# Performance work log

Hardware: AMD Instinct MI355X
Metric: run time of the kernel (lower is better)

## Reference

```python
import jax, jax.numpy as jnp
import numpy as np

N_HEAD_HALF = 8          # config.n_head // 2
LAMBDA_INIT = 0.2        # diff_lambda_init
RMS_EPS = 1.1920929e-07  # torch.finfo(float32).eps (F.rms_norm default)
ROPE_BASE = 10000.0


def setup_inputs() -> dict:
    key = jax.random.key(0)
    ks = jax.random.split(key, 9)
    B, T, C = 2, 2048, 2048
    HD = C // N_HEAD_HALF  # 256
    s = 0.02
    return {
        "x": jax.random.normal(ks[0], (B, T, C), jnp.float32),
        "wq": jax.random.normal(ks[1], (C, C), jnp.float32) * s,
        "wk": jax.random.normal(ks[2], (C, C), jnp.float32) * s,
        "wv": jax.random.normal(ks[3], (C, C), jnp.float32) * s,
        "wo": jax.random.normal(ks[4], (C, C), jnp.float32) * s,
        "lq1": jax.random.normal(ks[5], (HD,), jnp.float32) * 0.1,
        "lk1": jax.random.normal(ks[6], (HD,), jnp.float32) * 0.1,
        "lq2": jax.random.normal(ks[7], (HD,), jnp.float32) * 0.1,
        "lk2": jax.random.normal(ks[8], (HD,), jnp.float32) * 0.1,
    }


def _rms_norm(x):
    var = jnp.mean(x * x, axis=-1, keepdims=True)
    return x * jax.lax.rsqrt(var + RMS_EPS)


def _rotary(x):
    # Faithful to original bug: positions run along axis 1 (the HEAD axis),
    # since Rotary is applied after transpose(1,2). x: (B, NH, T, D)
    d = x.shape[-1]
    inv_freq = (1.0 / ROPE_BASE) ** (jnp.arange(0, d, 2, dtype=jnp.float32) / d)
    t = jnp.arange(x.shape[1], dtype=jnp.float32)
    freqs = jnp.outer(t, inv_freq)                      # (NH, d/2)
    cos = jnp.cos(freqs)[None, :, None, :]
    sin = jnp.sin(freqs)[None, :, None, :]
    x1, x2 = jnp.split(x, 2, axis=-1)
    return jnp.concatenate((x1 * cos + x2 * sin, -x1 * sin + x2 * cos), axis=-1)


def _causal_attn(q, k, v, scale):
    # q,k: (B,NH,T,Dh)  v: (B,NH,T,HD)
    T = q.shape[2]
    s = jnp.einsum("bhqd,bhkd->bhqk", q, k) * scale
    mask = jnp.tril(jnp.ones((T, T), dtype=bool))
    s = jnp.where(mask, s, jnp.float32(-jnp.inf))
    p = jax.nn.softmax(s, axis=-1)
    return jnp.einsum("bhqk,bhkd->bhqd", p, v)


def reference(x, wq, wk, wv, wo, lq1, lk1, lq2, lk2):
    B, T, C = x.shape
    NH = N_HEAD_HALF
    HD = C // NH
    HH = HD // 2

    lam1 = jnp.exp(jnp.sum(lq1 * lk1))
    lam2 = jnp.exp(jnp.sum(lq2 * lk2))
    lam = lam1 - lam2 + LAMBDA_INIT

    q = (x @ wq.T).reshape(B, T, NH, 2, HH).transpose(0, 2, 1, 3, 4)
    k = (x @ wk.T).reshape(B, T, NH, 2, HH).transpose(0, 2, 1, 3, 4)
    v = (x @ wv.T).reshape(B, T, NH, HD).transpose(0, 2, 1, 3)

    q1 = _rotary(_rms_norm(q[..., 0, :]))
    q2 = _rotary(_rms_norm(q[..., 1, :]))
    k1 = _rotary(_rms_norm(k[..., 0, :]))
    k2 = _rotary(_rms_norm(k[..., 1, :]))

    scale = 1.0 / jnp.sqrt(jnp.float32(HH))
    y = _causal_attn(q1, k1, v, scale) - lam * _causal_attn(q2, k2, v, scale)

    y = y.transpose(0, 2, 1, 3).reshape(B, T, C)
    y = (y @ wo.T) * (1.0 - LAMBDA_INIT)
    return y
```

## Files before the change

### kernel.cpp

```cpp
#include <hip/hip_runtime.h>
#include <hip/hip_bf16.h>

using bf16 = __hip_bfloat16;
typedef __bf16 bf16x8_t __attribute__((ext_vector_type(8)));
typedef __bf16 bf16x4_t __attribute__((ext_vector_type(4)));
typedef float f32x4  __attribute__((ext_vector_type(4)));
typedef float f32x16 __attribute__((ext_vector_type(16)));

#define AS1 __attribute__((address_space(1)))
#define AS3 __attribute__((address_space(3)))

__device__ __forceinline__ void gll16(const void* g, void* l) {
  __builtin_amdgcn_global_load_lds((const AS1 void*)g, (AS3 void*)l, 16u, 0, 0u);
}

__device__ __forceinline__ __bf16 tobf(float f) {
  bf16 h = __float2bfloat16(f);
  return __builtin_bit_cast(__bf16, h);
}

__global__ __launch_bounds__(256) void k_cvt(
    const float* __restrict__ x,  const float* __restrict__ wq,
    const float* __restrict__ wk, const float* __restrict__ wv,
    const float* __restrict__ wo,
    bf16* __restrict__ xb,  bf16* __restrict__ wqb, bf16* __restrict__ wkb,
    bf16* __restrict__ wvb, bf16* __restrict__ wob) {
  size_t id = (size_t)blockIdx.x * 256 + threadIdx.x;
  const float* s; bf16* d; size_t off;
  if (id < 2097152) { s = x; d = xb; off = id; }
  else {
    size_t r = id - 2097152;
    unsigned w = (unsigned)(r >> 20);
    off = r & 1048575u;
    s = (w == 0) ? wq : (w == 1) ? wk : (w == 2) ? wv : wo;
    d = (w == 0) ? wqb : (w == 1) ? wkb : (w == 2) ? wvb : wob;
  }
  const float4 v = ((const float4*)s)[off];
  bf16x4_t o = { tobf(v.x), tobf(v.y), tobf(v.z), tobf(v.w) };
  *(bf16x4_t*)(d + off * 4) = o;
}

__global__ __launch_bounds__(256) void k_lam(
    const float* __restrict__ lq1, const float* __restrict__ lk1,
    const float* __restrict__ lq2, const float* __restrict__ lk2,
    float* __restrict__ lam) {
  __shared__ float r1[4], r2[4];
  int t = threadIdx.x;
  float a = lq1[t] * lk1[t];
  float b = lq2[t] * lk2[t];
#pragma unroll
  for (int s = 1; s < 64; s <<= 1) { a += __shfl_xor(a, s); b += __shfl_xor(b, s); }
  if ((t & 63) == 0) { r1[t >> 6] = a; r2[t >> 6] = b; }
  __syncthreads();
  if (t == 0) {
    float s1 = r1[0] + r1[1] + r1[2] + r1[3];
    float s2 = r2[0] + r2[1] + r2[2] + r2[3];
    *lam = expf(s1) - expf(s2) + 0.2f;
  }
}

template<bool SWAP>
__device__ __forceinline__ void gemm_core(
    const bf16* __restrict__ A, const bf16* __restrict__ Bm,
    int m0, int n0, bf16* lA, bf16* lB, f32x4 (&acc)[4][4]) {
  const int tid  = threadIdx.x;
  const int lane = tid & 63;
  const int g    = lane >> 4;
  const int l15  = lane & 15;
  const int l7   = lane & 7;
  const int wave = tid >> 6;
  const int wm   = (wave >> 1) * 64;
  const int wn   = (wave & 1) * 64;

  int srow[4], ssc[4];
#pragma unroll
  for (int j = 0; j < 4; ++j) {
    int id = tid + j * 256;
    srow[j] = id >> 3;
    ssc[j]  = (id & 7) ^ (srow[j] & 7);
  }

  for (int k0 = 0; k0 < 2048; k0 += 64) {
    __syncthreads();
#pragma unroll
    for (int j = 0; j < 4; ++j) {
      int id = tid + j * 256;
      gll16(A  + (size_t)(m0 + srow[j]) * 2048 + k0 + ssc[j] * 8, lA + id * 8);
      gll16(Bm + (size_t)(n0 + srow[j]) * 2048 + k0 + ssc[j] * 8, lB + id * 8);
    }
    __syncthreads();
#pragma unroll
    for (int ks = 0; ks < 2; ++ks) {
      const int pc = (ks * 4 + g) ^ l7;
      bf16x8_t af[4], bfr[4];
#pragma unroll
      for (int mt = 0; mt < 4; ++mt)
        af[mt] = *(const bf16x8_t*)(lA + (wm + mt * 16 + l15) * 64 + pc * 8);
#pragma unroll
      for (int nt = 0; nt < 4; ++nt)
        bfr[nt] = *(const bf16x8_t*)(lB + (wn + nt * 16 + l15) * 64 + pc * 8);
#pragma unroll
      for (int mt = 0; mt < 4; ++mt)
#pragma unroll
        for (int nt = 0; nt < 4; ++nt) {
          if (SWAP)
            acc[mt][nt] = __builtin_amdgcn_mfma_f32_16x16x32_bf16(
                bfr[nt], af[mt], acc[mt][nt], 0, 0, 0);
          else
            acc[mt][nt] = __builtin_amdgcn_mfma_f32_16x16x32_bf16(
                af[mt], bfr[nt], acc[mt][nt], 0, 0, 0);
        }
    }
  }
}

__global__ __launch_bounds__(256) void k_gemm_qkv(
    const bf16* __restrict__ xb,
    const bf16* __restrict__ wqb, const bf16* __restrict__ wkb,
    const bf16* __restrict__ wvb,
    bf16* __restrict__ q1, bf16* __restrict__ q2,
    bf16* __restrict__ k1, bf16* __restrict__ k2,
    bf16* __restrict__ vt) {
  __shared__ __align__(16) bf16 lA[128 * 64];
  __shared__ __align__(16) bf16 lB[128 * 64];
  __shared__ float lCs[64], lSn[64];
  const int z  = blockIdx.z;
  const int m0 = blockIdx.y * 128, n0 = blockIdx.x * 128;
  const int tid = threadIdx.x;
  const int lane = tid & 63, wave = tid >> 6;
  const int g = lane >> 4, l15 = lane & 15, l7 = lane & 7;

  if (z < 2) {
    const bf16* Bm = z ? wkb : wqb;
    f32x4 acc[2][8] = {};

    int srow[4], ssc[4];
#pragma unroll
    for (int j = 0; j < 4; ++j) {
      int id = tid + j * 256;
      srow[j] = id >> 3;
      ssc[j]  = (id & 7) ^ (srow[j] & 7);
    }
    for (int k0 = 0; k0 < 2048; k0 += 64) {
      __syncthreads();
#pragma unroll
      for (int j = 0; j < 4; ++j) {
        int id = tid + j * 256;
        gll16(xb + (size_t)(m0 + srow[j]) * 2048 + k0 + ssc[j] * 8, lA + id * 8);
        gll16(Bm + (size_t)(n0 + srow[j]) * 2048 + k0 + ssc[j] * 8, lB + id * 8);
      }
      __syncthreads();
#pragma unroll
      for (int ks = 0; ks < 2; ++ks) {
        const int pc = (ks * 4 + g) ^ l7;
        bf16x8_t af[2], bfr[8];
#pragma unroll
        for (int mt = 0; mt < 2; ++mt)
          af[mt] = *(const bf16x8_t*)(lA + (wave * 32 + mt * 16 + l15) * 64 + pc * 8);
#pragma unroll
        for (int nt = 0; nt < 8; ++nt)
          bfr[nt] = *(const bf16x8_t*)(lB + (nt * 16 + l15) * 64 + pc * 8);
#pragma unroll
        for (int mt = 0; mt < 2; ++mt)
#pragma unroll
          for (int nt = 0; nt < 8; ++nt)
            acc[mt][nt] = __builtin_amdgcn_mfma_f32_16x16x32_bf16(
                bfr[nt], af[mt], acc[mt][nt], 0, 0, 0);
      }
    }

    const int nh = n0 >> 8, p = (n0 >> 7) & 1;
    __syncthreads();
    if (tid < 64) {
      float fr = exp2f(-(float)tid * 0.20762050593045951f);
      float sn, cs;
      sincosf((float)nh * fr, &sn, &cs);
      lCs[tid] = cs; lSn[tid] = sn;
    }
    __syncthreads();
    bf16* dst = z ? (p ? k2 : k1) : (p ? q2 : q1);
#pragma unroll
    for (int mt = 0; mt < 2; ++mt) {
      float ss = 0.f;
#pragma unroll
      for (int nt = 0; nt < 8; ++nt)
#pragma unroll
        for (int r = 0; r < 4; ++r) ss += acc[mt][nt][r] * acc[mt][nt][r];
      ss += __shfl_xor(ss, 16);
      ss += __shfl_xor(ss, 32);
      const float inv = rsqrtf(ss * (1.0f / 128.0f) + 1.1920929e-07f);
      const int tok = m0 + wave * 32 + mt * 16 + l15;
      const size_t base = ((size_t)tok * 8 + nh) * 128;
#pragma unroll
      for (int nt4 = 0; nt4 < 4; ++nt4) {
        const int jb = nt4 * 16 + 4 * g;
        bf16x4_t o1v, o2v;
#pragma unroll
        for (int r = 0; r < 4; ++r) {
          float cs = lCs[jb + r], sn = lSn[jb + r];
          float x1 = acc[mt][nt4][r] * inv;
          float x2 = acc[mt][nt4 + 4][r] * inv;
          o1v[r] = tobf(x1 * cs + x2 * sn);
          o2v[r] = tobf(x2 * cs - x1 * sn);
        }
        *(bf16x4_t*)(dst + base + jb)      = o1v;
        *(bf16x4_t*)(dst + base + jb + 64) = o2v;
      }
    }
  } else {
    f32x4 acc[4][4] = {};
    gemm_core<false>(xb, wvb, m0, n0, lA, lB, acc);
    const int wm = (wave >> 1) * 64, wn = (wave & 1) * 64;
#pragma unroll
    for (int mt = 0; mt < 4; ++mt)
#pragma unroll
      for (int nt = 0; nt < 4; ++nt) {
        int rb  = m0 + wm + mt * 16 + 4 * g;
        int col = n0 + wn + nt * 16 + l15;
        int nh = col >> 8, hd = col & 255;
        int b = rb >> 11, t = rb & 2047;
        bf16x4_t pv;
#pragma unroll
        for (int r = 0; r < 4; ++r) pv[r] = tobf(acc[mt][nt][r]);
        *(bf16x4_t*)(vt + ((size_t)((b * 8 + nh) * 256 + hd)) * 2048 + t) = pv;
      }
  }
}

__global__ __launch_bounds__(256) void k_gemm_out(
    const bf16* __restrict__ yb, const bf16* __restrict__ wob,
    float* __restrict__ outp) {
  __shared__ __align__(16) bf16 lA[128 * 64];
  __shared__ __align__(16) bf16 lB[128 * 64];
  const int m0 = blockIdx.y * 128, n0 = blockIdx.x * 128;
  f32x4 acc[4][4] = {};
  gemm_core<true>(yb, wob, m0, n0, lA, lB, acc);
  const int lane = threadIdx.x & 63, wave = threadIdx.x >> 6;
  const int g = lane >> 4, l15 = lane & 15;
  const int wm = (wave >> 1) * 64, wn = (wave & 1) * 64;
#pragma unroll
  for (int mt = 0; mt < 4; ++mt)
#pragma unroll
    for (int nt = 0; nt < 4; ++nt) {
      int row = m0 + wm + mt * 16 + l15;
      int col = n0 + wn + nt * 16 + 4 * g;
      f32x4 v;
#pragma unroll
      for (int r = 0; r < 4; ++r) v[r] = acc[mt][nt][r] * 0.8f;
      *(f32x4*)(outp + (size_t)row * 2048 + col) = v;
    }
}

__global__ __launch_bounds__(256, 1) void k_flash(
    const bf16* __restrict__ q1b, const bf16* __restrict__ q2b,
    const bf16* __restrict__ k1b, const bf16* __restrict__ k2b,
    const bf16* __restrict__ vtb, const float* __restrict__ lamp,
    bf16* __restrict__ yb) {
  __shared__ __align__(16) bf16 smem[65536];
  const int tid  = threadIdx.x;
  const int lane = tid & 63, wave = tid >> 6;
  const int pair = blockIdx.x;
  const int bh = blockIdx.y;
  const int b = bh >> 3, nh = bh & 7;
  const int at = wave & 1, qg = wave >> 1;
  const int l31 = lane & 31, g5 = lane >> 5, l7 = lane & 7;
  const float scale = 0.08838834764831845f;
  const float lam = *lamp;

  auto stage = [&](int kt, int buf) {
    bf16* dst = smem + buf * 32768;
    const int k0 = kt * 64;
#pragma unroll
    for (int it = 0; it < 4; ++it) {
      int id = tid + it * 256;
      int row = id >> 4, c = id & 15;
      int sc = (c & 8) | ((c & 7) ^ (row & 7));
      size_t goff = ((size_t)(b * 2048 + k0 + row) * 8 + nh) * 128 + sc * 8;
      gll16(k1b + goff, dst + id * 8);
      gll16(k2b + goff, dst + 8192 + id * 8);
    }
#pragma unroll
    for (int it = 0; it < 8; ++it) {
      int id = tid + it * 256;
      int row = id >> 3, c = id & 7;
      int sc = c ^ (row & 7);
      gll16(vtb + ((size_t)(bh * 256 + row)) * 2048 + k0 + sc * 8,
            dst + 16384 + id * 8);
    }
  };

  bf16x8_t qf[8];
  auto loadQ = [&](int qt) {
    int qglob = qt * 64 + qg * 32 + l31;
    const bf16* qp = (at ? q2b : q1b) +
                     ((size_t)(b * 2048 + qglob) * 8 + nh) * 128 + g5 * 8;
#pragma unroll
    for (int ks = 0; ks < 8; ++ks) qf[ks] = *(const bf16x8_t*)(qp + ks * 16);
  };

  f32x16 O[8];
  float mrun, lrun;
  auto resetO = [&]() {
#pragma unroll
    for (int i = 0; i < 8; ++i)
#pragma unroll
      for (int j = 0; j < 16; ++j) O[i][j] = 0.f;
    mrun = -1e30f; lrun = 0.f;
  };

  auto step = [&](int kt, int buf, int qt) {
    const bf16* lk = smem + buf * 32768 + (at ? 8192 : 0);
    const bf16* lv = smem + buf * 32768 + 16384;
    const int k0 = kt * 64;
    const int qglob = qt * 64 + qg * 32 + l31;

    f32x16 s0, s1;
#pragma unroll
    for (int j = 0; j < 16; ++j) { s0[j] = 0.f; s1[j] = 0.f; }
#pragma unroll
    for (int ks = 0; ks < 8; ++ks) {
      int cl = ks * 2 + g5;
      int pc = (cl & 8) | ((cl & 7) ^ l7);
      bf16x8_t a0 = *(const bf16x8_t*)(lk + l31 * 128 + pc * 8);
      bf16x8_t a1 = *(const bf16x8_t*)(lk + (32 + l31) * 128 + pc * 8);
      s0 = __builtin_amdgcn_mfma_f32_32x32x16_bf16(a0, qf[ks], s0, 0, 0, 0);
      s1 = __builtin_amdgcn_mfma_f32_32x32x16_bf16(a1, qf[ks], s1, 0, 0, 0);
    }

    const bool diag = (kt == qt);
    float rmax = -3.0e38f;
#pragma unroll
    for (int r = 0; r < 16; ++r) {
      int key0 = k0 + (r & 3) + 8 * (r >> 2) + 4 * g5;
      float v0 = s0[r] * scale;
      float v1 = s1[r] * scale;
      if (diag) {
        if (key0 > qglob)      v0 = -1e30f;
        if (key0 + 32 > qglob) v1 = -1e30f;
      }
      s0[r] = v0; s1[r] = v1;
      rmax = fmaxf(rmax, fmaxf(v0, v1));
    }
    rmax = fmaxf(rmax, __shfl_xor(rmax, 32));
    float mnew = fmaxf(mrun, rmax);
    float alpha = __expf(mrun - mnew);
    float psum = 0.f;
#pragma unroll
    for (int r = 0; r < 16; ++r) {
      float p0 = __expf(s0[r] - mnew);
      float p1 = __expf(s1[r] - mnew);
      s0[r] = p0; s1[r] = p1;
      psum += p0 + p1;
    }
    psum += __shfl_xor(psum, 32);
    lrun = lrun * alpha + psum;
    mrun = mnew;
#pragma unroll
    for (int i = 0; i < 8; ++i) O[i] *= alpha;

#pragma unroll
    for (int sl = 0; sl < 4; ++sl) {
      const int h = sl & 1;
      bf16x4_t lo, hi;
#pragma unroll
      for (int j = 0; j < 4; ++j) {
        float vl = (sl < 2) ? s0[h * 8 + j]     : s1[h * 8 + j];
        float vh = (sl < 2) ? s0[h * 8 + 4 + j] : s1[h * 8 + 4 + j];
        lo[j] = tobf(vl); hi[j] = tobf(vh);
      }
      bf16x4_t send = g5 ? lo : hi;
      int2 si = __builtin_bit_cast(int2, send);
      int2 ri;
      ri.x = __shfl_xor(si.x, 32);
      ri.y = __shfl_xor(si.y, 32);
      bf16x4_t recv = __builtin_bit_cast(bf16x4_t, ri);
      bf16x4_t f0 = g5 ? recv : lo;
      bf16x4_t f1 = g5 ? hi : recv;
      bf16x8_t pf = { f0[0], f0[1], f0[2], f0[3], f1[0], f1[1], f1[2], f1[3] };

      const int cl = sl * 2 + g5;
#pragma unroll
      for (int mt = 0; mt < 8; ++mt) {
        bf16x8_t vf = *(const bf16x8_t*)(lv + (mt * 32 + l31) * 64 + (cl ^ l7) * 8);
        O[mt] = __builtin_amdgcn_mfma_f32_32x32x16_bf16(vf, pf, O[mt], 0, 0, 0);
      }
    }
  };

  auto finish = [&](int qt, bf16* cb) {
    const int qglob = qt * 64 + qg * 32 + l31;
    const float invl = 1.f / lrun;
    __syncthreads();
    if (at) {
      const float f = lam * invl;
#pragma unroll
      for (int mt = 0; mt < 8; ++mt)
#pragma unroll
        for (int rq = 0; rq < 4; ++rq) {
          int hd = mt * 32 + 8 * rq + 4 * g5;
          bf16x4_t pv;
#pragma unroll
          for (int i = 0; i < 4; ++i) pv[i] = tobf(O[mt][rq * 4 + i] * f);
          *(bf16x4_t*)(cb + (size_t)(qg * 32 + l31) * 264 + hd) = pv;
        }
    }
    __syncthreads();
    if (!at) {
#pragma unroll
      for (int mt = 0; mt < 8; ++mt)
#pragma unroll
        for (int rq = 0; rq < 4; ++rq) {
          int hd = mt * 32 + 8 * rq + 4 * g5;
          bf16x4_t o2 = *(const bf16x4_t*)(cb + (size_t)(qg * 32 + l31) * 264 + hd);
          bf16x4_t pv;
#pragma unroll
          for (int i = 0; i < 4; ++i)
            pv[i] = tobf(O[mt][rq * 4 + i] * invl - (float)o2[i]);
          *(bf16x4_t*)(yb + (size_t)(b * 2048 + qglob) * 2048 + nh * 256 + hd) = pv;
        }
    }
  };

  const int qtB = 31 - pair, qtA = pair;

  loadQ(qtB);
  resetO();
  stage(0, 0);
  for (int kt = 0; kt <= qtB; ++kt) {
    __syncthreads();
    if (kt < qtB) stage(kt + 1, (kt + 1) & 1);
    else          stage(0, (kt + 1) & 1);
    step(kt, kt & 1, qtB);
  }
  finish(qtB, smem + (qtB & 1) * 32768);

  loadQ(qtA);
  resetO();
  for (int kt = 0; kt <= qtA; ++kt) {
    __syncthreads();
    if (kt < qtA) stage(kt + 1, (qtB + kt + 2) & 1);
    step(kt, (qtB + 1 + kt) & 1, qtA);
  }
  finish(qtA, smem + 32768);
}

extern "C" void kernel_launch(void* const* d_in, const int* in_sizes, int n_in,
                              void* d_out, int out_size, void* d_ws, size_t ws_size,
                              hipStream_t stream) {
  (void)in_sizes; (void)n_in; (void)out_size; (void)ws_size;
  const float* x   = (const float*)d_in[0];
  const float* wq  = (const float*)d_in[1];
  const float* wk  = (const float*)d_in[2];
  const float* wv  = (const float*)d_in[3];
  const float* wo  = (const float*)d_in[4];
  const float* lq1 = (const float*)d_in[5];
  const float* lk1 = (const float*)d_in[6];
  const float* lq2 = (const float*)d_in[7];
  const float* lk2 = (const float*)d_in[8];
  float* out = (float*)d_out;

  char* p = (char*)d_ws;
  float* lam = (float*)p;            p += 256;
  bf16* xb  = (bf16*)p;              p += (size_t)4096 * 2048 * 2;
  bf16* wqb = (bf16*)p;              p += (size_t)2048 * 2048 * 2;
  bf16* wkb = (bf16*)p;              p += (size_t)2048 * 2048 * 2;
  bf16* wvb = (bf16*)p;              p += (size_t)2048 * 2048 * 2;
  bf16* wob = (bf16*)p;              p += (size_t)2048 * 2048 * 2;
  bf16* vt  = (bf16*)p;              p += (size_t)4096 * 2048 * 2;
  bf16* q1b = (bf16*)p;              p += (size_t)4096 * 1024 * 2;
  bf16* q2b = (bf16*)p;              p += (size_t)4096 * 1024 * 2;
  bf16* k1b = (bf16*)p;              p += (size_t)4096 * 1024 * 2;
  bf16* k2b = (bf16*)p;              p += (size_t)4096 * 1024 * 2;
  bf16* yb  = (bf16*)p;              p += (size_t)4096 * 2048 * 2;

  k_cvt<<<24576, 256, 0, stream>>>(x, wq, wk, wv, wo, xb, wqb, wkb, wvb, wob);
  k_lam<<<1, 256, 0, stream>>>(lq1, lk1, lq2, lk2, lam);
  k_gemm_qkv<<<dim3(16, 32, 3), 256, 0, stream>>>(xb, wqb, wkb, wvb,
                                                  q1b, q2b, k1b, k2b, vt);
  k_flash<<<dim3(16, 16), 256, 0, stream>>>(q1b, q2b, k1b, k2b, vt, lam, yb);
  k_gemm_out<<<dim3(16, 32), 256, 0, stream>>>(yb, wob, out);
}
```

Baseline: 428.4 us.

## Use 3-stage LDS ring pipeline with 128x256 tiles and 512-thread GEMM blocks

Replaces the single-buffered load-then-compute GEMM loop with a 3-slot LDS ring that prefetches two k-tiles ahead, using vmcnt-based waits and a single barrier per step. Tiles grow to 128x256 with 8 waves per block, and s_setprio is raised around the MFMA bursts. In the QKV kernel each block now covers a full head, so the RMS norm is split across wave pairs and combined through shared memory. The aim is to hide global-load latency and cut barrier overhead. The cost is larger LDS use (about 144KB per block), which may limit occupancy.

New measurement: 453.1 us. +5.8%, slower.

```diff
diff --git a/kernel.cpp b/kernel.cpp
--- a/kernel.cpp
+++ b/kernel.cpp
@@ -59,147 +59,144 @@
   }
 }
 
+__device__ __forceinline__ void stage_ring(
+    const bf16* __restrict__ A, const bf16* __restrict__ B,
+    int m0, int n0, int k0, bf16* slot) {
+  const int tid = threadIdx.x;
+#pragma unroll
+  for (int j = 0; j < 2; ++j) {
+    int id = tid + j * 512;
+    int row = id >> 3, c = id & 7, sc = c ^ (row & 7);
+    gll16(A + (size_t)(m0 + row) * 2048 + k0 + sc * 8, slot + id * 8);
+  }
+#pragma unroll
+  for (int j = 0; j < 4; ++j) {
+    int id = tid + j * 512;
+    int row = id >> 3, c = id & 7, sc = c ^ (row & 7);
+    gll16(B + (size_t)(n0 + row) * 2048 + k0 + sc * 8, slot + 8192 + id * 8);
+  }
+}
+
 template<bool SWAP>
-__device__ __forceinline__ void gemm_core(
-    const bf16* __restrict__ A, const bf16* __restrict__ Bm,
-    int m0, int n0, bf16* lA, bf16* lB, f32x4 (&acc)[4][4]) {
+__device__ __forceinline__ void ring_gemm(
+    const bf16* __restrict__ A, const bf16* __restrict__ B,
+    int m0, int n0, bf16 (*ring)[24576], f32x4 (&acc)[4][4],
+    const int (&bfrow)[4]) {
   const int tid  = threadIdx.x;
   const int lane = tid & 63;
-  const int g    = lane >> 4;
-  const int l15  = lane & 15;
-  const int l7   = lane & 7;
-  const int wave = tid >> 6;
-  const int wm   = (wave >> 1) * 64;
-  const int wn   = (wave & 1) * 64;
-
-  int srow[4], ssc[4];
-#pragma unroll
-  for (int j = 0; j < 4; ++j) {
-    int id = tid + j * 256;
-    srow[j] = id >> 3;
-    ssc[j]  = (id & 7) ^ (srow[j] & 7);
-  }
-
-  for (int k0 = 0; k0 < 2048; k0 += 64) {
-    __syncthreads();
-#pragma unroll
-    for (int j = 0; j < 4; ++j) {
-      int id = tid + j * 256;
-      gll16(A  + (size_t)(m0 + srow[j]) * 2048 + k0 + ssc[j] * 8, lA + id * 8);
-      gll16(Bm + (size_t)(n0 + srow[j]) * 2048 + k0 + ssc[j] * 8, lB + id * 8);
-    }
-    __syncthreads();
+  const int g = lane >> 4, l15 = lane & 15, l7 = lane & 7;
+  const int wm = tid >> 8;
+
+  stage_ring(A, B, m0, n0, 0,  ring[0]);
+  stage_ring(A, B, m0, n0, 64, ring[1]);
+  asm volatile("s_waitcnt vmcnt(6)\n\ts_barrier" ::: "memory");
+
+  int s = 0;
+  for (int k = 0; k < 32; ++k) {
+    if (k < 30) {
+      int sp = s + 2; if (sp >= 3) sp -= 3;
+      stage_ring(A, B, m0, n0, (k + 2) * 64, ring[sp]);
+    }
+    const bf16* lA = ring[s];
+    const bf16* lB = ring[s] + 8192;
 #pragma unroll
     for (int ks = 0; ks < 2; ++ks) {
-      const int pc = (ks * 4 + g) ^ l7;
-      bf16x8_t af[4], bfr[4];
+      const int pc = ((ks * 4 + g) ^ l7) * 8;
+      bf16x8_t af[4], bv[4];
 #pragma unroll
       for (int mt = 0; mt < 4; ++mt)
-        af[mt] = *(const bf16x8_t*)(lA + (wm + mt * 16 + l15) * 64 + pc * 8);
+        af[mt] = *(const bf16x8_t*)(lA + (wm * 64 + mt * 16 + l15) * 64 + pc);
 #pragma unroll
       for (int nt = 0; nt < 4; ++nt)
-        bfr[nt] = *(const bf16x8_t*)(lB + (wn + nt * 16 + l15) * 64 + pc * 8);
+        bv[nt] = *(const bf16x8_t*)(lB + (bfrow[nt] + l15) * 64 + pc);
+      __builtin_amdgcn_s_setprio(1);
 #pragma unroll
       for (int mt = 0; mt < 4; ++mt)
 #pragma unroll
         for (int nt = 0; nt < 4; ++nt) {
           if (SWAP)
             acc[mt][nt] = __builtin_amdgcn_mfma_f32_16x16x32_bf16(
-                bfr[nt], af[mt], acc[mt][nt], 0, 0, 0);
+                bv[nt], af[mt], acc[mt][nt], 0, 0, 0);
           else
             acc[mt][nt] = __builtin_amdgcn_mfma_f32_16x16x32_bf16(
-                af[mt], bfr[nt], acc[mt][nt], 0, 0, 0);
+                af[mt], bv[nt], acc[mt][nt], 0, 0, 0);
         }
-    }
-  }
-}
-
-__global__ __launch_bounds__(256) void k_gemm_qkv(
+      __builtin_amdgcn_s_setprio(0);
+    }
+    if (k < 30)       asm volatile("s_waitcnt vmcnt(6)\n\ts_barrier" ::: "memory");
+    else if (k == 30) asm volatile("s_waitcnt vmcnt(0)\n\ts_barrier" ::: "memory");
+    s = (s == 2) ? 0 : s + 1;
+  }
+}
+
+__device__ __forceinline__ void make_bfrow(int wn, int (&bfrow)[4]) {
+  const int p = wn >> 1, j2 = wn & 1;
+#pragma unroll
+  for (int nt = 0; nt < 4; ++nt)
+    bfrow[nt] = p * 128 + j2 * 32 + (nt & 1) * 16 + (nt >> 1) * 64;
+}
+
+__global__ __launch_bounds__(512, 2) void k_gemm_qkv(
     const bf16* __restrict__ xb,
     const bf16* __restrict__ wqb, const bf16* __restrict__ wkb,
     const bf16* __restrict__ wvb,
     bf16* __restrict__ q1, bf16* __restrict__ q2,
     bf16* __restrict__ k1, bf16* __restrict__ k2,
     bf16* __restrict__ vt) {
-  __shared__ __align__(16) bf16 lA[128 * 64];
-  __shared__ __align__(16) bf16 lB[128 * 64];
+  __shared__ __align__(16) bf16 ring[3][24576];
+  __shared__ float ex[8][64];
   __shared__ float lCs[64], lSn[64];
   const int z  = blockIdx.z;
-  const int m0 = blockIdx.y * 128, n0 = blockIdx.x * 128;
-  const int tid = threadIdx.x;
-  const int lane = tid & 63, wave = tid >> 6;
-  const int g = lane >> 4, l15 = lane & 15, l7 = lane & 7;
+  const int m0 = blockIdx.y * 128, n0 = blockIdx.x * 256;
+  const int nh = blockIdx.x;
+  const int tid = threadIdx.x, lane = tid & 63, wave = tid >> 6;
+  const int wm = wave >> 2, wn = wave & 3;
+  const int g = lane >> 4, l15 = lane & 15;
+  const int p = wn >> 1, j2 = wn & 1;
+  int bfrow[4];
+  make_bfrow(wn, bfrow);
+  f32x4 acc[4][4] = {};
 
   if (z < 2) {
     const bf16* Bm = z ? wkb : wqb;
-    f32x4 acc[2][8] = {};
-
-    int srow[4], ssc[4];
-#pragma unroll
-    for (int j = 0; j < 4; ++j) {
-      int id = tid + j * 256;
-      srow[j] = id >> 3;
-      ssc[j]  = (id & 7) ^ (srow[j] & 7);
-    }
-    for (int k0 = 0; k0 < 2048; k0 += 64) {
-      __syncthreads();
-#pragma unroll
-      for (int j = 0; j < 4; ++j) {
-        int id = tid + j * 256;
-        gll16(xb + (size_t)(m0 + srow[j]) * 2048 + k0 + ssc[j] * 8, lA + id * 8);
-        gll16(Bm + (size_t)(n0 + srow[j]) * 2048 + k0 + ssc[j] * 8, lB + id * 8);
-      }
-      __syncthreads();
-#pragma unroll
-      for (int ks = 0; ks < 2; ++ks) {
-        const int pc = (ks * 4 + g) ^ l7;
-        bf16x8_t af[2], bfr[8];
-#pragma unroll
-        for (int mt = 0; mt < 2; ++mt)
-          af[mt] = *(const bf16x8_t*)(lA + (wave * 32 + mt * 16 + l15) * 64 + pc * 8);
-#pragma unroll
-        for (int nt = 0; nt < 8; ++nt)
-          bfr[nt] = *(const bf16x8_t*)(lB + (nt * 16 + l15) * 64 + pc * 8);
-#pragma unroll
-        for (int mt = 0; mt < 2; ++mt)
-#pragma unroll
-          for (int nt = 0; nt < 8; ++nt)
-            acc[mt][nt] = __builtin_amdgcn_mfma_f32_16x16x32_bf16(
-                bfr[nt], af[mt], acc[mt][nt], 0, 0, 0);
-      }
-    }
-
-    const int nh = n0 >> 8, p = (n0 >> 7) & 1;
-    __syncthreads();
+    ring_gemm<true>(xb, Bm, m0, n0, ring, acc, bfrow);
+
     if (tid < 64) {
       float fr = exp2f(-(float)tid * 0.20762050593045951f);
       float sn, cs;
       sincosf((float)nh * fr, &sn, &cs);
       lCs[tid] = cs; lSn[tid] = sn;
     }
-    __syncthreads();
-    bf16* dst = z ? (p ? k2 : k1) : (p ? q2 : q1);
-#pragma unroll
-    for (int mt = 0; mt < 2; ++mt) {
+    float ssown[4];
+#pragma unroll
+    for (int mt = 0; mt < 4; ++mt) {
       float ss = 0.f;
 #pragma unroll
-      for (int nt = 0; nt < 8; ++nt)
+      for (int nt = 0; nt < 4; ++nt)
 #pragma unroll
         for (int r = 0; r < 4; ++r) ss += acc[mt][nt][r] * acc[mt][nt][r];
       ss += __shfl_xor(ss, 16);
       ss += __shfl_xor(ss, 32);
-      const float inv = rsqrtf(ss * (1.0f / 128.0f) + 1.1920929e-07f);
-      const int tok = m0 + wave * 32 + mt * 16 + l15;
+      ssown[mt] = ss;
+      if (g == 0) ex[wave][mt * 16 + l15] = ss;
+    }
+    __syncthreads();
+    bf16* dst = z ? (p ? k2 : k1) : (p ? q2 : q1);
+#pragma unroll
+    for (int mt = 0; mt < 4; ++mt) {
+      const float sst = ssown[mt] + ex[wave ^ 1][mt * 16 + l15];
+      const float inv = rsqrtf(sst * (1.0f / 128.0f) + 1.1920929e-07f);
+      const int tok = m0 + wm * 64 + mt * 16 + l15;
       const size_t base = ((size_t)tok * 8 + nh) * 128;
 #pragma unroll
-      for (int nt4 = 0; nt4 < 4; ++nt4) {
-        const int jb = nt4 * 16 + 4 * g;
+      for (int nt2 = 0; nt2 < 2; ++nt2) {
+        const int jb = j2 * 32 + nt2 * 16 + 4 * g;
         bf16x4_t o1v, o2v;
 #pragma unroll
         for (int r = 0; r < 4; ++r) {
           float cs = lCs[jb + r], sn = lSn[jb + r];
-          float x1 = acc[mt][nt4][r] * inv;
-          float x2 = acc[mt][nt4 + 4][r] * inv;
+          float x1 = acc[mt][nt2][r] * inv;
+          float x2 = acc[mt][nt2 + 2][r] * inv;
           o1v[r] = tobf(x1 * cs + x2 * sn);
           o2v[r] = tobf(x2 * cs - x1 * sn);
         }
@@ -208,16 +205,13 @@
       }
     }
   } else {
-    f32x4 acc[4][4] = {};
-    gemm_core<false>(xb, wvb, m0, n0, lA, lB, acc);
-    const int wm = (wave >> 1) * 64, wn = (wave & 1) * 64;
+    ring_gemm<false>(xb, wvb, m0, n0, ring, acc, bfrow);
 #pragma unroll
     for (int mt = 0; mt < 4; ++mt)
 #pragma unroll
       for (int nt = 0; nt < 4; ++nt) {
-        int rb  = m0 + wm + mt * 16 + 4 * g;
-        int col = n0 + wn + nt * 16 + l15;
-        int nh = col >> 8, hd = col & 255;
+        int rb = m0 + wm * 64 + mt * 16 + 4 * g;
+        int hd = bfrow[nt] + l15;
         int b = rb >> 11, t = rb & 2047;
         bf16x4_t pv;
 #pragma unroll
@@ -227,23 +221,24 @@
   }
 }
 
-__global__ __launch_bounds__(256) void k_gemm_out(
+__global__ __launch_bounds__(512, 2) void k_gemm_out(
     const bf16* __restrict__ yb, const bf16* __restrict__ wob,
     float* __restrict__ outp) {
-  __shared__ __align__(16) bf16 lA[128 * 64];
-  __shared__ __align__(16) bf16 lB[128 * 64];
-  const int m0 = blockIdx.y * 128, n0 = blockIdx.x * 128;
+  __shared__ __align__(16) bf16 ring[3][24576];
+  const int m0 = blockIdx.y * 128, n0 = blockIdx.x * 256;
+  const int tid = threadIdx.x, lane = tid & 63, wave = tid >> 6;
+  const int wm = wave >> 2, wn = wave & 3;
+  const int g = lane >> 4, l15 = lane & 15;
+  int bfrow[4];
+  make_bfrow(wn, bfrow);
   f32x4 acc[4][4] = {};
-  gemm_core<true>(yb, wob, m0, n0, lA, lB, acc);
-  const int lane = threadIdx.x & 63, wave = threadIdx.x >> 6;
-  const int g = lane >> 4, l15 = lane & 15;
-  const int wm = (wave >> 1) * 64, wn = (wave & 1) * 64;
+  ring_gemm<true>(yb, wob, m0, n0, ring, acc, bfrow);
 #pragma unroll
   for (int mt = 0; mt < 4; ++mt)
 #pragma unroll
     for (int nt = 0; nt < 4; ++nt) {
-      int row = m0 + wm + mt * 16 + l15;
-      int col = n0 + wn + nt * 16 + 4 * g;
+      int row = m0 + wm * 64 + mt * 16 + l15;
+      int col = n0 + bfrow[nt] + 4 * g;
       f32x4 v;
 #pragma unroll
       for (int r = 0; r < 4; ++r) v[r] = acc[mt][nt][r] * 0.8f;
@@ -475,8 +470,8 @@
 
   k_cvt<<<24576, 256, 0, stream>>>(x, wq, wk, wv, wo, xb, wqb, wkb, wvb, wob);
   k_lam<<<1, 256, 0, stream>>>(lq1, lk1, lq2, lk2, lam);
-  k_gemm_qkv<<<dim3(16, 32, 3), 256, 0, stream>>>(xb, wqb, wkb, wvb,
-                                                  q1b, q2b, k1b, k2b, vt);
+  k_gemm_qkv<<<dim3(8, 32, 3), 512, 0, stream>>>(xb, wqb, wkb, wvb,
+                                                 q1b, q2b, k1b, k2b, vt);
   k_flash<<<dim3(16, 16), 256, 0, stream>>>(q1b, q2b, k1b, k2b, vt, lam, yb);
-  k_gemm_out<<<dim3(16, 32), 256, 0, stream>>>(yb, wob, out);
-}
+  k_gemm_out<<<dim3(8, 32), 512, 0, stream>>>(yb, wob, out);
+}
```

## Rewrite QKV GEMM with 256x256 tiles, 8 waves and double-buffered LDS pipeline

Applied to the files above, without the earlier changes.

Replaces the 128x128 single-buffered QKV projection GEMM with a 256x256 tile kernel using 512 threads. It double-buffers A/B tiles in LDS with interleaved async global-to-LDS loads, explicit barriers and MFMA priority boosting so loads overlap compute. RMS norm now combines per-head row sums across waves through shared memory, since each wave holds only part of a head row. It uses much more LDS per block and fewer blocks (384), which risks lower occupancy and under-filling the CUs.

Measured after the change: 434.0 us. Within noise of the previous version (+1.3%).

```diff
diff --git a/kernel.cpp b/kernel.cpp
--- a/kernel.cpp
+++ b/kernel.cpp
@@ -59,6 +59,211 @@
   }
 }
 
+#define MFMA16(a, b, c) __builtin_amdgcn_mfma_f32_16x16x32_bf16(a, b, c, 0, 0, 0)
+
+template<bool SWAP>
+__device__ __forceinline__ void gemm256(
+    const bf16* __restrict__ A, const bf16* __restrict__ B,
+    int m0, int n0, bf16* lds, f32x4 (&acc)[8][4]) {
+  const int tid = threadIdx.x, lane = tid & 63;
+  const int wave = tid >> 6, m = wave >> 2, n = wave & 3;
+  const int g = lane >> 4, l15 = lane & 15, l7 = lane & 7;
+
+  const int sid0 = tid, sid1 = tid + 512;
+  const int sr0 = sid0 >> 3, sc0 = (sid0 & 7) ^ (sr0 & 7);
+  const int sr1 = sid1 >> 3, sc1 = (sid1 & 7) ^ (sr1 & 7);
+
+  auto stageA = [&](int t, int h) {
+    bf16* d = lds + ((size_t)((t & 1) * 2 + h)) * 8192;
+    gll16(A + (size_t)(m0 + h * 128 + sr0) * 2048 + t * 64 + sc0 * 8, d + sid0 * 8);
+    gll16(A + (size_t)(m0 + h * 128 + sr1) * 2048 + t * 64 + sc1 * 8, d + sid1 * 8);
+  };
+  auto stageB = [&](int t, int h) {
+    bf16* d = lds + 32768 + ((size_t)((t & 1) * 2 + h)) * 8192;
+    gll16(B + (size_t)(n0 + h * 128 + sr0) * 2048 + t * 64 + sc0 * 8, d + sid0 * 8);
+    gll16(B + (size_t)(n0 + h * 128 + sr1) * 2048 + t * 64 + sc1 * 8, d + sid1 * 8);
+  };
+
+  stageA(0, 0); stageB(0, 0); stageB(0, 1); stageA(0, 1);
+  stageA(1, 0); stageB(1, 0); stageB(1, 1);
+  asm volatile("s_waitcnt vmcnt(6)\n\ts_barrier" ::: "memory");
+
+  for (int t = 0; t < 32; ++t) {
+    const bf16* lA0 = lds + ((size_t)((t & 1) * 2 + 0)) * 8192;
+    const bf16* lA1 = lds + ((size_t)((t & 1) * 2 + 1)) * 8192;
+    const bf16* lB0 = lds + 32768 + ((size_t)((t & 1) * 2 + 0)) * 8192;
+    const bf16* lB1 = lds + 32768 + ((size_t)((t & 1) * 2 + 1)) * 8192;
+    bf16x8_t afl[4][2], afh[4][2], bvl[2][2], bvh[2][2];
+
+#pragma unroll
+    for (int ks = 0; ks < 2; ++ks) {
+      const int pc = ((ks * 4 + g) ^ l7) * 8;
+#pragma unroll
+      for (int rf = 0; rf < 4; ++rf)
+        afl[rf][ks] = *(const bf16x8_t*)(lA0 + (m * 64 + rf * 16 + l15) * 64 + pc);
+#pragma unroll
+      for (int cf = 0; cf < 2; ++cf)
+        bvl[cf][ks] = *(const bf16x8_t*)(lB0 + (cf * 64 + n * 16 + l15) * 64 + pc);
+    }
+    if (t + 1 < 32) stageA(t + 1, 1);
+    asm volatile("s_barrier" ::: "memory");
+    __builtin_amdgcn_s_setprio(1);
+#pragma unroll
+    for (int ks = 0; ks < 2; ++ks)
+#pragma unroll
+      for (int rf = 0; rf < 4; ++rf)
+#pragma unroll
+        for (int cf = 0; cf < 2; ++cf)
+          acc[rf][cf] = SWAP ? MFMA16(bvl[cf][ks], afl[rf][ks], acc[rf][cf])
+                             : MFMA16(afl[rf][ks], bvl[cf][ks], acc[rf][cf]);
+    __builtin_amdgcn_s_setprio(0);
+    asm volatile("s_barrier" ::: "memory");
+
+#pragma unroll
+    for (int ks = 0; ks < 2; ++ks) {
+      const int pc = ((ks * 4 + g) ^ l7) * 8;
+#pragma unroll
+      for (int cf = 0; cf < 2; ++cf)
+        bvh[cf][ks] = *(const bf16x8_t*)(lB1 + (cf * 64 + n * 16 + l15) * 64 + pc);
+    }
+    if (t + 2 < 32) stageA(t + 2, 0);
+    asm volatile("s_barrier" ::: "memory");
+    __builtin_amdgcn_s_setprio(1);
+#pragma unroll
+    for (int ks = 0; ks < 2; ++ks)
+#pragma unroll
+      for (int rf = 0; rf < 4; ++rf)
+#pragma unroll
+        for (int cf = 0; cf < 2; ++cf)
+          acc[rf][cf + 2] = SWAP ? MFMA16(bvh[cf][ks], afl[rf][ks], acc[rf][cf + 2])
+                                 : MFMA16(afl[rf][ks], bvh[cf][ks], acc[rf][cf + 2]);
+    __builtin_amdgcn_s_setprio(0);
+    asm volatile("s_barrier" ::: "memory");
+
+#pragma unroll
+    for (int ks = 0; ks < 2; ++ks) {
+      const int pc = ((ks * 4 + g) ^ l7) * 8;
+#pragma unroll
+      for (int rf = 0; rf < 4; ++rf)
+        afh[rf][ks] = *(const bf16x8_t*)(lA1 + (m * 64 + rf * 16 + l15) * 64 + pc);
+    }
+    if (t + 2 < 32) stageB(t + 2, 0);
+    asm volatile("s_barrier" ::: "memory");
+    __builtin_amdgcn_s_setprio(1);
+#pragma unroll
+    for (int ks = 0; ks < 2; ++ks)
+#pragma unroll
+      for (int rf = 0; rf < 4; ++rf)
+#pragma unroll
+        for (int cf = 0; cf < 2; ++cf)
+          acc[rf + 4][cf + 2] = SWAP ? MFMA16(bvh[cf][ks], afh[rf][ks], acc[rf + 4][cf + 2])
+                                     : MFMA16(afh[rf][ks], bvh[cf][ks], acc[rf + 4][cf + 2]);
+    __builtin_amdgcn_s_setprio(0);
+    asm volatile("s_barrier" ::: "memory");
+
+    if (t + 2 < 32) stageB(t + 2, 1);
+    asm volatile("s_barrier" ::: "memory");
+    __builtin_amdgcn_s_setprio(1);
+#pragma unroll
+    for (int ks = 0; ks < 2; ++ks)
+#pragma unroll
+      for (int rf = 0; rf < 4; ++rf)
+#pragma unroll
+        for (int cf = 0; cf < 2; ++cf)
+          acc[rf + 4][cf] = SWAP ? MFMA16(bvl[cf][ks], afh[rf][ks], acc[rf + 4][cf])
+                                 : MFMA16(afh[rf][ks], bvl[cf][ks], acc[rf + 4][cf]);
+    __builtin_amdgcn_s_setprio(0);
+    if (t < 30)      asm volatile("s_waitcnt vmcnt(6)\n\ts_barrier" ::: "memory");
+    else             asm volatile("s_waitcnt vmcnt(0)\n\ts_barrier" ::: "memory");
+  }
+}
+
+__global__ __launch_bounds__(512, 2) void k_gemm_qkv(
+    const bf16* __restrict__ xb,
+    const bf16* __restrict__ wqb, const bf16* __restrict__ wkb,
+    const bf16* __restrict__ wvb,
+    bf16* __restrict__ q1, bf16* __restrict__ q2,
+    bf16* __restrict__ k1, bf16* __restrict__ k2,
+    bf16* __restrict__ vt) {
+  __shared__ __align__(16) bf16 lds[65536];
+  __shared__ float exs[2][4][256];
+  __shared__ float lCs[64], lSn[64];
+  const int z  = blockIdx.z;
+  const int m0 = blockIdx.y * 256, n0 = blockIdx.x * 256;
+  const int nh = blockIdx.x;
+  const int tid = threadIdx.x, lane = tid & 63, wave = tid >> 6;
+  const int m = wave >> 2, n = wave & 3;
+  const int g = lane >> 4, l15 = lane & 15;
+  f32x4 acc[8][4] = {};
+
+  if (z < 2) {
+    if (tid < 64) {
+      float fr = exp2f(-(float)tid * 0.20762050593045951f);
+      float sn, cs;
+      sincosf((float)nh * fr, &sn, &cs);
+      lCs[tid] = cs; lSn[tid] = sn;
+    }
+    const bf16* Bm = z ? wkb : wqb;
+    gemm256<true>(xb, Bm, m0, n0, lds, acc);
+
+#pragma unroll
+    for (int rf = 0; rf < 8; ++rf) {
+      float s0 = 0.f, s1 = 0.f;
+#pragma unroll
+      for (int r = 0; r < 4; ++r) {
+        s0 += acc[rf][0][r] * acc[rf][0][r] + acc[rf][1][r] * acc[rf][1][r];
+        s1 += acc[rf][2][r] * acc[rf][2][r] + acc[rf][3][r] * acc[rf][3][r];
+      }
+      s0 += __shfl_xor(s0, 16); s0 += __shfl_xor(s0, 32);
+      s1 += __shfl_xor(s1, 16); s1 += __shfl_xor(s1, 32);
+      const int rrow = (rf >> 2) * 128 + m * 64 + (rf & 3) * 16 + l15;
+      if (g == 0) { exs[0][n][rrow] = s0; exs[1][n][rrow] = s1; }
+    }
+    __syncthreads();
+    bf16* dst1 = z ? k1 : q1;
+    bf16* dst2 = z ? k2 : q2;
+    const int j = n * 16 + 4 * g;
+#pragma unroll
+    for (int rf = 0; rf < 8; ++rf) {
+      const int rrow = (rf >> 2) * 128 + m * 64 + (rf & 3) * 16 + l15;
+      const float t0 = exs[0][0][rrow] + exs[0][1][rrow] + exs[0][2][rrow] + exs[0][3][rrow];
+      const float t1 = exs[1][0][rrow] + exs[1][1][rrow] + exs[1][2][rrow] + exs[1][3][rrow];
+      const float inv0 = rsqrtf(t0 * (1.0f / 128.0f) + 1.1920929e-07f);
+      const float inv1 = rsqrtf(t1 * (1.0f / 128.0f) + 1.1920929e-07f);
+      const size_t base = ((size_t)(m0 + rrow) * 8 + nh) * 128;
+      bf16x4_t o1a, o2a, o1b, o2b;
+#pragma unroll
+      for (int r = 0; r < 4; ++r) {
+        const float cs = lCs[j + r], sn = lSn[j + r];
+        float x1 = acc[rf][0][r] * inv0, x2 = acc[rf][1][r] * inv0;
+        o1a[r] = tobf(x1 * cs + x2 * sn);
+        o2a[r] = tobf(x2 * cs - x1 * sn);
+        x1 = acc[rf][2][r] * inv1; x2 = acc[rf][3][r] * inv1;
+        o1b[r] = tobf(x1 * cs + x2 * sn);
+        o2b[r] = tobf(x2 * cs - x1 * sn);
+      }
+      *(bf16x4_t*)(dst1 + base + j)      = o1a;
+      *(bf16x4_t*)(dst1 + base + j + 64) = o2a;
+      *(bf16x4_t*)(dst2 + base + j)      = o1b;
+      *(bf16x4_t*)(dst2 + base + j + 64) = o2b;
+    }
+  } else {
+    gemm256<false>(xb, wvb, m0, n0, lds, acc);
+#pragma unroll
+    for (int rf = 0; rf < 8; ++rf)
+#pragma unroll
+      for (int cf = 0; cf < 4; ++cf) {
+        const int rb = m0 + (rf >> 2) * 128 + m * 64 + (rf & 3) * 16 + 4 * g;
+        const int hd = (cf & 1) * 64 + (cf >> 1) * 128 + n * 16 + l15;
+        const int b = rb >> 11, t = rb & 2047;
+        bf16x4_t pv;
+#pragma unroll
+        for (int r = 0; r < 4; ++r) pv[r] = tobf(acc[rf][cf][r]);
+        *(bf16x4_t*)(vt + ((size_t)((b * 8 + nh) * 256 + hd)) * 2048 + t) = pv;
+      }
+  }
+}
+
 template<bool SWAP>
 __device__ __forceinline__ void gemm_core(
     const bf16* __restrict__ A, const bf16* __restrict__ Bm,
@@ -104,126 +309,11 @@
 #pragma unroll
         for (int nt = 0; nt < 4; ++nt) {
           if (SWAP)
-            acc[mt][nt] = __builtin_amdgcn_mfma_f32_16x16x32_bf16(
-                bfr[nt], af[mt], acc[mt][nt], 0, 0, 0);
+            acc[mt][nt] = MFMA16(bfr[nt], af[mt], acc[mt][nt]);
           else
-            acc[mt][nt] = __builtin_amdgcn_mfma_f32_16x16x32_bf16(
-                af[mt], bfr[nt], acc[mt][nt], 0, 0, 0);
+            acc[mt][nt] = MFMA16(af[mt], bfr[nt], acc[mt][nt]);
         }
     }
-  }
-}
-
-__global__ __launch_bounds__(256) void k_gemm_qkv(
-    const bf16* __restrict__ xb,
-    const bf16* __restrict__ wqb, const bf16* __restrict__ wkb,
-    const bf16* __restrict__ wvb,
-    bf16* __restrict__ q1, bf16* __restrict__ q2,
-    bf16* __restrict__ k1, bf16* __restrict__ k2,
-    bf16* __restrict__ vt) {
-  __shared__ __align__(16) bf16 lA[128 * 64];
-  __shared__ __align__(16) bf16 lB[128 * 64];
-  __shared__ float lCs[64], lSn[64];
-  const int z  = blockIdx.z;
-  const int m0 = blockIdx.y * 128, n0 = blockIdx.x * 128;
-  const int tid = threadIdx.x;
-  const int lane = tid & 63, wave = tid >> 6;
-  const int g = lane >> 4, l15 = lane & 15, l7 = lane & 7;
-
-  if (z < 2) {
-    const bf16* Bm = z ? wkb : wqb;
-    f32x4 acc[2][8] = {};
-
-    int srow[4], ssc[4];
-#pragma unroll
-    for (int j = 0; j < 4; ++j) {
-      int id = tid + j * 256;
-      srow[j] = id >> 3;
-      ssc[j]  = (id & 7) ^ (srow[j] & 7);
-    }
-    for (int k0 = 0; k0 < 2048; k0 += 64) {
-      __syncthreads();
-#pragma unroll
-      for (int j = 0; j < 4; ++j) {
-        int id = tid + j * 256;
-        gll16(xb + (size_t)(m0 + srow[j]) * 2048 + k0 + ssc[j] * 8, lA + id * 8);
-        gll16(Bm + (size_t)(n0 + srow[j]) * 2048 + k0 + ssc[j] * 8, lB + id * 8);
-      }
-      __syncthreads();
-#pragma unroll
-      for (int ks = 0; ks < 2; ++ks) {
-        const int pc = (ks * 4 + g) ^ l7;
-        bf16x8_t af[2], bfr[8];
-#pragma unroll
-        for (int mt = 0; mt < 2; ++mt)
-          af[mt] = *(const bf16x8_t*)(lA + (wave * 32 + mt * 16 + l15) * 64 + pc * 8);
-#pragma unroll
-        for (int nt = 0; nt < 8; ++nt)
-          bfr[nt] = *(const bf16x8_t*)(lB + (nt * 16 + l15) * 64 + pc * 8);
-#pragma unroll
-        for (int mt = 0; mt < 2; ++mt)
-#pragma unroll
-          for (int nt = 0; nt < 8; ++nt)
-            acc[mt][nt] = __builtin_amdgcn_mfma_f32_16x16x32_bf16(
-                bfr[nt], af[mt], acc[mt][nt], 0, 0, 0);
-      }
-    }
-
-    const int nh = n0 >> 8, p = (n0 >> 7) & 1;
-    __syncthreads();
-    if (tid < 64) {
-      float fr = exp2f(-(float)tid * 0.20762050593045951f);
-      float sn, cs;
-      sincosf((float)nh * fr, &sn, &cs);
-      lCs[tid] = cs; lSn[tid] = sn;
-    }
-    __syncthreads();
-    bf16* dst = z ? (p ? k2 : k1) : (p ? q2 : q1);
-#pragma unroll
-    for (int mt = 0; mt < 2; ++mt) {
-      float ss = 0.f;
-#pragma unroll
-      for (int nt = 0; nt < 8; ++nt)
-#pragma unroll
-        for (int r = 0; r < 4; ++r) ss += acc[mt][nt][r] * acc[mt][nt][r];
-      ss += __shfl_xor(ss, 16);
-      ss += __shfl_xor(ss, 32);
-      const float inv = rsqrtf(ss * (1.0f / 128.0f) + 1.1920929e-07f);
-      const int tok = m0 + wave * 32 + mt * 16 + l15;
-      const size_t base = ((size_t)tok * 8 + nh) * 128;
-#pragma unroll
-      for (int nt4 = 0; nt4 < 4; ++nt4) {
-        const int jb = nt4 * 16 + 4 * g;
-        bf16x4_t o1v, o2v;
-#pragma unroll
-        for (int r = 0; r < 4; ++r) {
-          float cs = lCs[jb + r], sn = lSn[jb + r];
-          float x1 = acc[mt][nt4][r] * inv;
-          float x2 = acc[mt][nt4 + 4][r] * inv;
-          o1v[r] = tobf(x1 * cs + x2 * sn);
-          o2v[r] = tobf(x2 * cs - x1 * sn);
-        }
-        *(bf16x4_t*)(dst + base + jb)      = o1v;
-        *(bf16x4_t*)(dst + base + jb + 64) = o2v;
-      }
-    }
-  } else {
-    f32x4 acc[4][4] = {};
-    gemm_core<false>(xb, wvb, m0, n0, lA, lB, acc);
-    const int wm = (wave >> 1) * 64, wn = (wave & 1) * 64;
-#pragma unroll
-    for (int mt = 0; mt < 4; ++mt)
-#pragma unroll
-      for (int nt = 0; nt < 4; ++nt) {
-        int rb  = m0 + wm + mt * 16 + 4 * g;
-        int col = n0 + wn + nt * 16 + l15;
-        int nh = col >> 8, hd = col & 255;
-        int b = rb >> 11, t = rb & 2047;
-        bf16x4_t pv;
-#pragma unroll
-        for (int r = 0; r < 4; ++r) pv[r] = tobf(acc[mt][nt][r]);
-        *(bf16x4_t*)(vt + ((size_t)((b * 8 + nh) * 256 + hd)) * 2048 + t) = pv;
-      }
   }
 }
 
@@ -475,8 +565,8 @@
 
   k_cvt<<<24576, 256, 0, stream>>>(x, wq, wk, wv, wo, xb, wqb, wkb, wvb, wob);
   k_lam<<<1, 256, 0, stream>>>(lq1, lk1, lq2, lk2, lam);
-  k_gemm_qkv<<<dim3(16, 32, 3), 256, 0, stream>>>(xb, wqb, wkb, wvb,
-                                                  q1b, q2b, k1b, k2b, vt);
+  k_gemm_qkv<<<dim3(8, 16, 3), 512, 0, stream>>>(xb, wqb, wkb, wvb,
+                                                 q1b, q2b, k1b, k2b, vt);
   k_flash<<<dim3(16, 16), 256, 0, stream>>>(q1b, q2b, k1b, k2b, vt, lam, yb);
   k_gemm_out<<<dim3(16, 32), 256, 0, stream>>>(yb, wob, out);
 }
```
